# Performance work log

Hardware: AMD Instinct MI355X
Metric: run time of the kernel (lower is better)

The kernel has to match this reference:

```python
import jax, jax.numpy as jnp
import numpy as np

B, D, K, P = 512, 2048, 128, 5

def setup_inputs() -> dict:
    key = jax.random.key(0)
    k1, k2 = jax.random.split(key)
    x = jax.random.normal(k1, (B, D), dtype=jnp.float32)
    theta = 0.05 * jax.random.normal(k2, (D, K, P), dtype=jnp.float32)
    log_weight_scale = jnp.zeros((K, P), dtype=jnp.float32)
    bias = -jnp.ones((K,), dtype=jnp.float32)  # layer inits bias to -1
    return {"x": x, "theta": theta, "log_weight_scale": log_weight_scale, "bias": bias}

def reference(x, theta, log_weight_scale, bias):
    b = x.shape[0]
    # weight-normalized kernel: [D, K, P]
    norm = jnp.sqrt(jnp.sum(theta * theta, axis=0))            # [K, P]
    kernel = theta * (jnp.exp(log_weight_scale) / norm)[None]  # [D, K, P]
    actv = jnp.einsum('bd,dkp->bkp', x, kernel)                # [B, K, P]
    # pairwise L1 over P: [B, K, B]
    diff = jnp.abs(actv[:, :, :, None] - jnp.transpose(actv, (1, 2, 0))[None])  # [B,K,P,B]
    abs_dif = jnp.sum(diff, axis=2) + 1e6 * jnp.eye(b, dtype=x.dtype)[:, None, :]
    f = jnp.sum(jnp.exp(-abs_dif), axis=2) + bias[None, :]     # [B, K]
    return jnp.concatenate([x, f], axis=1)                     # [B, D+K]
```

## Files before the change

kernel.cpp:

```cpp
#include <hip/hip_runtime.h>
#include <math.h>

#define BSZ 512
#define DD 2048
#define KK 128
#define PP 5
#define NCOL (KK * PP)
#define OUTW (DD + KK)
#define LOG2E 1.4426950408889634f

#define KSPLIT 16
#define GM 64
#define GN 64
#define GK (DD / KSPLIT)
#define GBK 32
#define QSPLIT 8

#define WS_NORM 0
#define WS_ACTV (WS_NORM + NCOL)
#define WS_FPART (WS_ACTV + BSZ * NCOL)
#define WS_PART (WS_FPART + QSPLIT * KK * BSZ)

__global__ __launch_bounds__(256) void norm_kernel(const float* __restrict__ theta,
                                                   float* __restrict__ norm) {
    __shared__ float partial[32][8];
    const int t   = threadIdx.x;
    const int c8  = blockIdx.x * 8;
    const int col = c8 + (t & 7);
    const int g   = t >> 3;
    const float* p = theta + (size_t)g * NCOL + col;
    float s = 0.f;
#pragma unroll
    for (int j = 0; j < 64; ++j) {
        float v = p[(size_t)j * 32 * NCOL];
        s += v * v;
    }
    partial[g][t & 7] = s;
    __syncthreads();
    if (t < 8) {
        float acc = 0.f;
#pragma unroll
        for (int gg = 0; gg < 32; ++gg) acc += partial[gg][t];
        norm[c8 + t] = acc;
    }
}

__global__ __launch_bounds__(256) void gemm_kernel(const float* __restrict__ x,
                                                   const float* __restrict__ theta,
                                                   float* __restrict__ part,
                                                   float* __restrict__ out) {
    __shared__ float xT[GBK][GM];

    if (blockIdx.z == KSPLIT) {
        const int bid = blockIdx.y * (NCOL / GN) + blockIdx.x;
        for (int i = bid * 256 + threadIdx.x; i < BSZ * (DD / 4); i += 80 * 256) {
            int r = i >> 9;
            int c = i & 511;
            float4 v = *(const float4*)&x[(size_t)r * DD + c * 4];
            *(float4*)&out[(size_t)r * OUTW + c * 4] = v;
        }
        return;
    }

    const int t    = threadIdx.x;
    const int lane = t & 63;
    const int wave = t >> 6;
    const int m    = blockIdx.y * GM + lane;
    const int kz   = blockIdx.z * GK;
    const int nw = __builtin_amdgcn_readfirstlane(blockIdx.x * GN + wave * 16);

    const float* xrow = x + (size_t)m * DD;

    float acc[16] = {};

    float4 v0 = *(const float4*)&xrow[kz + wave * 8];
    float4 v1 = *(const float4*)&xrow[kz + wave * 8 + 4];

    for (int kc = kz; kc < kz + GK; kc += GBK) {
        __syncthreads();
        xT[wave * 8 + 0][lane] = v0.x;
        xT[wave * 8 + 1][lane] = v0.y;
        xT[wave * 8 + 2][lane] = v0.z;
        xT[wave * 8 + 3][lane] = v0.w;
        xT[wave * 8 + 4][lane] = v1.x;
        xT[wave * 8 + 5][lane] = v1.y;
        xT[wave * 8 + 6][lane] = v1.z;
        xT[wave * 8 + 7][lane] = v1.w;
        __syncthreads();

        if (kc + GBK < kz + GK) {
            v0 = *(const float4*)&xrow[kc + GBK + wave * 8];
            v1 = *(const float4*)&xrow[kc + GBK + wave * 8 + 4];
        }

        const float* th = &theta[(size_t)kc * NCOL + nw];
#pragma unroll 4
        for (int kk = 0; kk < GBK; ++kk) {
            const float a = xT[kk][lane];
#pragma unroll
            for (int j = 0; j < 16; ++j)
                acc[j] += a * th[(size_t)kk * NCOL + j];
        }
    }

    float* dst = part + (size_t)blockIdx.z * (BSZ * NCOL) + (size_t)m * NCOL + nw;
    *(float4*)&dst[0]  = make_float4(acc[0],  acc[1],  acc[2],  acc[3]);
    *(float4*)&dst[4]  = make_float4(acc[4],  acc[5],  acc[6],  acc[7]);
    *(float4*)&dst[8]  = make_float4(acc[8],  acc[9],  acc[10], acc[11]);
    *(float4*)&dst[12] = make_float4(acc[12], acc[13], acc[14], acc[15]);
}

__global__ __launch_bounds__(256) void reduce_kernel(const float* __restrict__ part,
                                                     const float* __restrict__ norm,
                                                     const float* __restrict__ lws,
                                                     float* __restrict__ actv) {
    int i   = blockIdx.x * 256 + threadIdx.x;
    int col = i % NCOL;
    float s = 0.f;
#pragma unroll
    for (int q = 0; q < KSPLIT; ++q)
        s += part[(size_t)q * (BSZ * NCOL) + i];
    const float scale = __builtin_amdgcn_exp2f(lws[col] * LOG2E) *
                        __builtin_amdgcn_rsqf(norm[col]) * LOG2E;
    actv[i] = s * scale;
}

__global__ __launch_bounds__(128) void pairwise_kernel(const float* __restrict__ actv,
                                                       float* __restrict__ f_part) {
    const int k   = blockIdx.x;
    const int q   = blockIdx.y;
    const int tid = threadIdx.x;

    __shared__ float sB[64][8];

    for (int i = tid; i < 64 * PP; i += 128) {
        int r = i / PP;
        int p = i - r * PP;
        sB[r][p] = actv[(size_t)(q * 64 + r) * NCOL + k * PP + p];
    }

    float a[4][PP];
#pragma unroll
    for (int r = 0; r < 4; ++r) {
        const float* ap = &actv[(size_t)(tid + r * 128) * NCOL + k * PP];
#pragma unroll
        for (int p = 0; p < PP; ++p) a[r][p] = ap[p];
    }
    __syncthreads();

    float acc[4] = {0.f, 0.f, 0.f, 0.f};
#pragma unroll 2
    for (int j = 0; j < 64; ++j) {
        const float4 v  = *(const float4*)&sB[j][0];
        const float  v4 = sB[j][4];
#pragma unroll
        for (int r = 0; r < 4; ++r) {
            float s = fabsf(a[r][0] - v.x) + fabsf(a[r][1] - v.y) +
                      fabsf(a[r][2] - v.z) + fabsf(a[r][3] - v.w) +
                      fabsf(a[r][4] - v4);
            acc[r] += __builtin_amdgcn_exp2f(-s);
        }
    }

    float* fp = f_part + ((size_t)q * KK + k) * BSZ;
#pragma unroll
    for (int r = 0; r < 4; ++r)
        fp[tid + r * 128] = acc[r];
}

__global__ __launch_bounds__(256) void freduce_kernel(const float* __restrict__ f_part,
                                                      const float* __restrict__ bias,
                                                      float* __restrict__ out) {
    int i = blockIdx.x * 256 + threadIdx.x;
    int k = i >> 9;
    int b = i & 511;
    float s = 0.f;
#pragma unroll
    for (int q = 0; q < QSPLIT; ++q)
        s += f_part[((size_t)q * KK + k) * BSZ + b];
    out[(size_t)b * OUTW + DD + k] = s - 1.0f + bias[k];
}

extern "C" void kernel_launch(void* const* d_in, const int* in_sizes, int n_in,
                              void* d_out, int out_size, void* d_ws, size_t ws_size,
                              hipStream_t stream) {
    const float* x     = (const float*)d_in[0];
    const float* theta = (const float*)d_in[1];
    const float* lws   = (const float*)d_in[2];
    const float* bias  = (const float*)d_in[3];
    float* out = (float*)d_out;

    float* ws     = (float*)d_ws;
    float* norm   = ws + WS_NORM;
    float* actv   = ws + WS_ACTV;
    float* f_part = ws + WS_FPART;
    float* part   = ws + WS_PART;

    norm_kernel<<<80, 256, 0, stream>>>(theta, norm);
    gemm_kernel<<<dim3(NCOL / GN, BSZ / GM, KSPLIT + 1), 256, 0, stream>>>(x, theta, part, out);
    reduce_kernel<<<(BSZ * NCOL) / 256, 256, 0, stream>>>(part, norm, lws, actv);
    pairwise_kernel<<<dim3(KK, QSPLIT), 128, 0, stream>>>(actv, f_part);
    freduce_kernel<<<256, 256, 0, stream>>>(f_part, bias, out);
}
```

Measured before the change: 122.6 us.

## Convert GEMM operands to bf16 and compute with MFMA instructions

A prep kernel now computes the column norms and also converts x and a transposed copy of theta to bf16 in workspace. The GEMM is rewritten to use 16x16x32 bf16 MFMA instructions on LDS tiles, and the K-split drops from 16 to 8. This replaces the scalar fp32 FMA inner loop with matrix-core work and shrinks the partial-sum traffic. In exchange it adds a conversion pass over x and theta and lowers precision. Because the pairwise stage applies exp of summed L1 distances, the bf16 error could affect accuracy.

```diff
diff --git a/kernel.cpp b/kernel.cpp
--- a/kernel.cpp
+++ b/kernel.cpp
@@ -9,50 +9,106 @@
 #define OUTW (DD + KK)
 #define LOG2E 1.4426950408889634f
 
-#define KSPLIT 16
-#define GM 64
-#define GN 64
+#define KSPLIT 8
 #define GK (DD / KSPLIT)
-#define GBK 32
 #define QSPLIT 8
+
+typedef __attribute__((ext_vector_type(8))) short bf16x8;
+typedef __attribute__((ext_vector_type(4))) float f32x4;
 
 #define WS_NORM 0
 #define WS_ACTV (WS_NORM + NCOL)
 #define WS_FPART (WS_ACTV + BSZ * NCOL)
-#define WS_PART (WS_FPART + QSPLIT * KK * BSZ)
-
-__global__ __launch_bounds__(256) void norm_kernel(const float* __restrict__ theta,
-                                                   float* __restrict__ norm) {
+#define WS_XB (WS_FPART + QSPLIT * KK * BSZ)
+#define WS_THT (WS_XB + BSZ * DD / 2)
+#define WS_PART (WS_THT + NCOL * DD / 2)
+
+__device__ inline ushort f2b(float f) {
+    unsigned u = __float_as_uint(f);
+    u += 0x7FFF + ((u >> 16) & 1);
+    return (ushort)(u >> 16);
+}
+
+__global__ __launch_bounds__(256) void prep_kernel(const float* __restrict__ theta,
+                                                   const float* __restrict__ x,
+                                                   float* __restrict__ norm,
+                                                   ushort* __restrict__ thT,
+                                                   ushort* __restrict__ xb) {
     __shared__ float partial[32][8];
+    __shared__ ushort sT[64][68];
+
+    const int bid = blockIdx.x;
     const int t   = threadIdx.x;
-    const int c8  = blockIdx.x * 8;
-    const int col = c8 + (t & 7);
-    const int g   = t >> 3;
-    const float* p = theta + (size_t)g * NCOL + col;
-    float s = 0.f;
-#pragma unroll
-    for (int j = 0; j < 64; ++j) {
-        float v = p[(size_t)j * 32 * NCOL];
-        s += v * v;
-    }
-    partial[g][t & 7] = s;
-    __syncthreads();
-    if (t < 8) {
-        float acc = 0.f;
-#pragma unroll
-        for (int gg = 0; gg < 32; ++gg) acc += partial[gg][t];
-        norm[c8 + t] = acc;
-    }
-}
-
-__global__ __launch_bounds__(256) void gemm_kernel(const float* __restrict__ x,
-                                                   const float* __restrict__ theta,
+
+    if (bid < 80) {
+        const int c8  = bid * 8;
+        const int col = c8 + (t & 7);
+        const int g   = t >> 3;
+        const float* p = theta + (size_t)g * NCOL + col;
+        float s = 0.f;
+#pragma unroll
+        for (int j = 0; j < 64; ++j) {
+            float v = p[(size_t)j * 32 * NCOL];
+            s += v * v;
+        }
+        partial[g][t & 7] = s;
+        __syncthreads();
+        if (t < 8) {
+            float acc = 0.f;
+#pragma unroll
+            for (int gg = 0; gg < 32; ++gg) acc += partial[gg][t];
+            norm[c8 + t] = acc;
+        }
+    } else if (bid < 400) {
+        const int tb    = bid - 80;
+        const int kz    = (tb & 31) * 64;
+        const int nz    = (tb >> 5) * 64;
+        const int c4    = t & 15;
+        const int rbase = t >> 4;
+#pragma unroll
+        for (int i = 0; i < 4; ++i) {
+            int r = rbase + i * 16;
+            float4 v = *(const float4*)&theta[(size_t)(kz + r) * NCOL + nz + c4 * 4];
+            sT[c4 * 4 + 0][r] = f2b(v.x);
+            sT[c4 * 4 + 1][r] = f2b(v.y);
+            sT[c4 * 4 + 2][r] = f2b(v.z);
+            sT[c4 * 4 + 3][r] = f2b(v.w);
+        }
+        __syncthreads();
+#pragma unroll
+        for (int i = 0; i < 2; ++i) {
+            int slot = t + i * 256;
+            int rr   = slot >> 3;
+            int cc   = (slot & 7) * 8;
+            ushort4 w0 = *(const ushort4*)&sT[rr][cc];
+            ushort4 w1 = *(const ushort4*)&sT[rr][cc + 4];
+            ushort* dst = &thT[(size_t)(nz + rr) * DD + kz + cc];
+            *(ushort4*)&dst[0] = w0;
+            *(ushort4*)&dst[4] = w1;
+        }
+    } else {
+        const int b2 = bid - 400;
+#pragma unroll
+        for (int i = 0; i < 4; ++i) {
+            int base = b2 * 4096 + i * 1024 + t * 4;
+            float4 v = *(const float4*)&x[base];
+            ushort4 w;
+            w.x = f2b(v.x); w.y = f2b(v.y); w.z = f2b(v.z); w.w = f2b(v.w);
+            *(ushort4*)&xb[base] = w;
+        }
+    }
+}
+
+__global__ __launch_bounds__(256) void gemm_kernel(const ushort* __restrict__ xb,
+                                                   const ushort* __restrict__ thT,
                                                    float* __restrict__ part,
+                                                   const float* __restrict__ x,
                                                    float* __restrict__ out) {
-    __shared__ float xT[GBK][GM];
+    __shared__ ushort lA[64][136];
+    __shared__ ushort lB[64][136];
 
     if (blockIdx.z == KSPLIT) {
-        const int bid = blockIdx.y * (NCOL / GN) + blockIdx.x;
+        const int bid = blockIdx.y * 10 + blockIdx.x;
         for (int i = bid * 256 + threadIdx.x; i < BSZ * (DD / 4); i += 80 * 256) {
             int r = i >> 9;
             int c = i & 511;
@@ -65,49 +121,72 @@
     const int t    = threadIdx.x;
     const int lane = t & 63;
     const int wave = t >> 6;
-    const int m    = blockIdx.y * GM + lane;
+    const int bn   = blockIdx.x * 64;
+    const int bm   = blockIdx.y * 64;
     const int kz   = blockIdx.z * GK;
-    const int nw = __builtin_amdgcn_readfirstlane(blockIdx.x * GN + wave * 16);
-
-    const float* xrow = x + (size_t)m * DD;
-
-    float acc[16] = {};
-
-    float4 v0 = *(const float4*)&xrow[kz + wave * 8];
-    float4 v1 = *(const float4*)&xrow[kz + wave * 8 + 4];
-
-    for (int kc = kz; kc < kz + GK; kc += GBK) {
-        __syncthreads();
-        xT[wave * 8 + 0][lane] = v0.x;
-        xT[wave * 8 + 1][lane] = v0.y;
-        xT[wave * 8 + 2][lane] = v0.z;
-        xT[wave * 8 + 3][lane] = v0.w;
-        xT[wave * 8 + 4][lane] = v1.x;
-        xT[wave * 8 + 5][lane] = v1.y;
-        xT[wave * 8 + 6][lane] = v1.z;
-        xT[wave * 8 + 7][lane] = v1.w;
-        __syncthreads();
-
-        if (kc + GBK < kz + GK) {
-            v0 = *(const float4*)&xrow[kc + GBK + wave * 8];
-            v1 = *(const float4*)&xrow[kc + GBK + wave * 8 + 4];
-        }
-
-        const float* th = &theta[(size_t)kc * NCOL + nw];
-#pragma unroll 4
-        for (int kk = 0; kk < GBK; ++kk) {
-            const float a = xT[kk][lane];
-#pragma unroll
-            for (int j = 0; j < 16; ++j)
-                acc[j] += a * th[(size_t)kk * NCOL + j];
-        }
-    }
-
-    float* dst = part + (size_t)blockIdx.z * (BSZ * NCOL) + (size_t)m * NCOL + nw;
-    *(float4*)&dst[0]  = make_float4(acc[0],  acc[1],  acc[2],  acc[3]);
-    *(float4*)&dst[4]  = make_float4(acc[4],  acc[5],  acc[6],  acc[7]);
-    *(float4*)&dst[8]  = make_float4(acc[8],  acc[9],  acc[10], acc[11]);
-    *(float4*)&dst[12] = make_float4(acc[12], acc[13], acc[14], acc[15]);
+
+    const ushort* gA = xb  + (size_t)bm * DD + kz;
+    const ushort* gB = thT + (size_t)bn * DD + kz;
+
+    f32x4 acc[2][2] = {};
+
+    uint4 va[4], vb[4];
+#pragma unroll
+    for (int i = 0; i < 4; ++i) {
+        int slot = t + i * 256, rr = slot >> 4, ss = slot & 15;
+        va[i] = *(const uint4*)&gA[(size_t)rr * DD + ss * 8];
+        vb[i] = *(const uint4*)&gB[(size_t)rr * DD + ss * 8];
+    }
+
+    const int fr = lane & 15;
+    const int g  = lane >> 4;
+    const int mr = (wave >> 1) * 32 + fr;
+    const int nr = (wave & 1) * 32 + fr;
+
+#pragma unroll
+    for (int c = 0; c < 2; ++c) {
+        __syncthreads();
+#pragma unroll
+        for (int i = 0; i < 4; ++i) {
+            int slot = t + i * 256, rr = slot >> 4, ss = slot & 15;
+            *(uint4*)&lA[rr][ss * 8] = va[i];
+            *(uint4*)&lB[rr][ss * 8] = vb[i];
+        }
+        __syncthreads();
+        if (c == 0) {
+#pragma unroll
+            for (int i = 0; i < 4; ++i) {
+                int slot = t + i * 256, rr = slot >> 4, ss = slot & 15;
+                va[i] = *(const uint4*)&gA[(size_t)rr * DD + 128 + ss * 8];
+                vb[i] = *(const uint4*)&gB[(size_t)rr * DD + 128 + ss * 8];
+            }
+        }
+#pragma unroll
+        for (int ks = 0; ks < 4; ++ks) {
+            const int kc = ks * 32 + g * 8;
+            bf16x8 a0 = *(const bf16x8*)&lA[mr][kc];
+            bf16x8 a1 = *(const bf16x8*)&lA[mr + 16][kc];
+            bf16x8 b0 = *(const bf16x8*)&lB[nr][kc];
+            bf16x8 b1 = *(const bf16x8*)&lB[nr + 16][kc];
+            acc[0][0] = __builtin_amdgcn_mfma_f32_16x16x32_bf16(a0, b0, acc[0][0], 0, 0, 0);
+            acc[0][1] = __builtin_amdgcn_mfma_f32_16x16x32_bf16(a0, b1, acc[0][1], 0, 0, 0);
+            acc[1][0] = __builtin_amdgcn_mfma_f32_16x16x32_bf16(a1, b0, acc[1][0], 0, 0, 0);
+            acc[1][1] = __builtin_amdgcn_mfma_f32_16x16x32_bf16(a1, b1, acc[1][1], 0, 0, 0);
+        }
+    }
+
+    float* base = part + (size_t)blockIdx.z * (BSZ * NCOL);
+#pragma unroll
+    for (int mt = 0; mt < 2; ++mt)
+#pragma unroll
+        for (int nt = 0; nt < 2; ++nt) {
+            int row = bm + (wave >> 1) * 32 + mt * 16 + g * 4;
+            int col = bn + (wave & 1) * 32 + nt * 16 + fr;
+            float* dst = base + (size_t)row * NCOL + col;
+#pragma unroll
+            for (int reg = 0; reg < 4; ++reg)
+                dst[(size_t)reg * NCOL] = acc[mt][nt][reg];
+        }
 }
 
 __global__ __launch_bounds__(256) void reduce_kernel(const float* __restrict__ part,
@@ -194,10 +273,12 @@
     float* norm   = ws + WS_NORM;
     float* actv   = ws + WS_ACTV;
     float* f_part = ws + WS_FPART;
+    ushort* xb    = (ushort*)(ws + WS_XB);
+    ushort* thT   = (ushort*)(ws + WS_THT);
     float* part   = ws + WS_PART;
 
-    norm_kernel<<<80, 256, 0, stream>>>(theta, norm);
-    gemm_kernel<<<dim3(NCOL / GN, BSZ / GM, KSPLIT + 1), 256, 0, stream>>>(x, theta, part, out);
+    prep_kernel<<<656, 256, 0, stream>>>(theta, x, norm, thT, xb);
+    gemm_kernel<<<dim3(NCOL / 64, BSZ / 64, KSPLIT + 1), 256, 0, stream>>>(xb, thT, part, x, out);
     reduce_kernel<<<(BSZ * NCOL) / 256, 256, 0, stream>>>(part, norm, lws, actv);
     pairwise_kernel<<<dim3(KK, QSPLIT), 128, 0, stream>>>(actv, f_part);
     freduce_kernel<<<256, 256, 0, stream>>>(f_part, bias, out);
```

New measurement: 116.9 us. -4.7%, faster.
